# Performance work log

Measured on AMD Instinct MI355X. Metric: run time of the kernel, lower is better.

The kernel has to match this reference:

```python
import jax, jax.numpy as jnp
import numpy as np

L = 8          # curve control points per chunk (self.l)
TS = 256       # curve spatial resolution (self.ts)


def setup_inputs() -> dict:
    key = jax.random.key(0)
    k1, k2 = jax.random.split(key)
    # full-resolution input image, values in [0,1)
    x = jax.random.uniform(k1, (4, 3, 1024, 1024), dtype=jnp.float32)
    # predicted curve parameters: 9*L = 72 channels at TS x TS
    param = jax.random.normal(k2, (4, 72, TS, TS), dtype=jnp.float32)
    return {"x": x, "param": param}


def _grid_sample_3d(vol, gx, gy, gz):
    """F.grid_sample(vol, grid, 'bilinear', 'border', align_corners=True)
    vol: [B,C,D,Hc,Wc]; gx,gy,gz: [B,H,W] normalized coords in [-1,1].
    Returns [B,H,W,C] (channels last)."""
    B, C, D, Hc, Wc = vol.shape
    # align_corners=True unnormalization + border padding (clamp coords)
    ix = jnp.clip((gx + 1.0) * 0.5 * (Wc - 1), 0.0, Wc - 1)
    iy = jnp.clip((gy + 1.0) * 0.5 * (Hc - 1), 0.0, Hc - 1)
    iz = jnp.clip((gz + 1.0) * 0.5 * (D - 1), 0.0, D - 1)
    x0f, y0f, z0f = jnp.floor(ix), jnp.floor(iy), jnp.floor(iz)
    wx, wy, wz = ix - x0f, iy - y0f, iz - z0f
    x0 = x0f.astype(jnp.int32); x1 = jnp.minimum(x0 + 1, Wc - 1)
    y0 = y0f.astype(jnp.int32); y1 = jnp.minimum(y0 + 1, Hc - 1)
    z0 = z0f.astype(jnp.int32); z1 = jnp.minimum(z0 + 1, D - 1)
    vol_t = vol.transpose(0, 2, 3, 4, 1)  # [B,D,Hc,Wc,C]
    b = jnp.arange(B)[:, None, None]      # [B,1,1]
    out = jnp.zeros(gx.shape + (C,), dtype=vol.dtype)
    for zi, wz_ in ((z0, 1.0 - wz), (z1, wz)):
        for yi, wy_ in ((y0, 1.0 - wy), (y1, wy)):
            for xi, wx_ in ((x0, 1.0 - wx), (x1, wx)):
                w = (wz_ * wy_ * wx_)[..., None]          # [B,H,W,1]
                out = out + w * vol_t[b, zi, yi, xi]      # gather -> [B,H,W,C]
    return out


def reference(x, param):
    # eval-mode forward of Generator.mapping + tanh (param precomputed by CNN)
    B, _, H, W = x.shape
    Hc, Wc = param.shape[-2], param.shape[-1]
    # torch.stack(torch.chunk(param,3,dim=1),dim=1) == reshape [B,3,3L,Hc,Wc]
    curve = param.reshape(B, 3, 3 * L, Hc, Wc)
    coordh = jnp.linspace(-1.0, 1.0, H, dtype=x.dtype)[:, None]  # varies over H
    coordw = jnp.linspace(-1.0, 1.0, W, dtype=x.dtype)[None, :]  # varies over W
    gx = jnp.broadcast_to(coordw, (B, H, W))
    gy = jnp.broadcast_to(coordh, (B, H, W))
    out = jnp.zeros((B, H, W, 3), dtype=x.dtype)
    for i in range(3):  # three curve chunks, z-coordinate = i-th color channel
        curve_i = curve[:, :, i * L:(i + 1) * L]          # [B,3,L,Hc,Wc]
        out = out + _grid_sample_3d(curve_i, gx, gy, x[:, i])
    return jnp.tanh(out.transpose(0, 3, 1, 2))            # [B,3,H,W]
```

## Files before the change

### kernel.cpp

```cpp
#include <hip/hip_runtime.h>
#include <math.h>

#define IMG 1024
#define HW (IMG * IMG)
#define TS 256
#define CH_STRIDE (TS * TS)
#define PARAM_B_STRIDE (72 * CH_STRIDE)
#define S_CONST (255.0f / 1023.0f)

#define ROWS 6
#define CELLS 34
#define CELL_DW 73
#define ROW_DW (CELLS * CELL_DW)
#define LDS_DW (ROWS * ROW_DW)
#define RUNS (ROWS * 72)
#define STAGE_DW (RUNS * CELLS)

__global__ __launch_bounds__(1024, 8) void curve3d_fused(
    const float* __restrict__ x, const float* __restrict__ param,
    float* __restrict__ out)
{
    __shared__ float sh[LDS_DW];
    int blk = blockIdx.x;
    blk = (blk & 7) * 256 + (blk >> 3);
    int wt = blk & 7;
    int ht = (blk >> 3) & 63;
    int b  = blk >> 9;
    int tid = threadIdx.x;

    int w0 = wt * 128, h0 = ht * 16;
    int xb = (int)((float)w0 * S_CONST);
    int yb = (int)((float)h0 * S_CONST);

    int tw = tid & 127, th = tid >> 7;
    int w = w0 + tw;
    int ha = h0 + th;
    const float* xp = x + (size_t)b * 3 * HW + (size_t)ha * IMG + w;
    float xv[2][3];
#pragma unroll
    for (int i = 0; i < 3; ++i) {
        xv[0][i] = __builtin_nontemporal_load(xp + (size_t)i * HW);
        xv[1][i] = __builtin_nontemporal_load(xp + (size_t)i * HW + 8 * IMG);
    }

    const float* pb = param + (size_t)b * PARAM_B_STRIDE;
#pragma unroll
    for (int j = 0; j < 15; ++j) {
        int idx = tid + j * 1024;
        if (j < 14 || idx < STAGE_DW) {
            int run = idx / CELLS;
            int off = idx - run * CELLS;
            int row = run / 72;
            int ch  = run - row * 72;
            int ys = min(yb + row, 255);
            int xs = min(xb + off, 255);
            sh[row * ROW_DW + off * CELL_DW + ch] =
                pb[(size_t)ch * CH_STRIDE + ys * TS + xs];
        }
    }

    int zi[2][3]; float wz[2][3];
#pragma unroll
    for (int p = 0; p < 2; ++p)
#pragma unroll
        for (int i = 0; i < 3; ++i) {
            float f = fminf(fmaxf(fmaf(xv[p][i], 3.5f, 3.5f), 0.0f), 7.0f);
            int z = min((int)f, 6);
            zi[p][i] = z;
            wz[p][i] = f - (float)z;
        }

    __syncthreads();

    float ixf = (float)w * S_CONST; int x0 = (int)ixf; float wx = ixf - (float)x0;
    int cb0 = (x0 - xb) * CELL_DW;
    int cb1 = (min(x0 + 1, 255) - xb) * CELL_DW;
    float u0 = 1.0f - wx;

    float* op = out + (size_t)b * 3 * HW + (size_t)ha * IMG + w;

#pragma unroll
    for (int p = 0; p < 2; ++p) {
        int h = ha + p * 8;
        float iyf = (float)h * S_CONST; int y0 = (int)iyf; float wy = iyf - (float)y0;
        int rb0 = (y0 - yb) * ROW_DW;
        int rb1 = (min(y0 + 1, 255) - yb) * ROW_DW;
        float v0 = 1.0f - wy;
        float wcs[4] = {v0 * u0, v0 * wx, wy * u0, wy * wx};
        int bofs[4] = {rb0 + cb0, rb0 + cb1, rb1 + cb0, rb1 + cb1};
        float* opp = op + (size_t)(p * 8) * IMG;
#pragma unroll
        for (int c = 0; c < 3; ++c) {
            float acc = 0.0f;
#pragma unroll
            for (int i = 0; i < 3; ++i) {
                int off = (c * 3 + i) * 8 + zi[p][i];
                float wzi = wz[p][i];
#pragma unroll
                for (int k = 0; k < 4; ++k) {
                    float2 v;
                    __builtin_memcpy(&v, &sh[bofs[k] + off], 8);
                    float wb = wcs[k] * wzi;
                    float wa = wcs[k] - wb;
                    acc = fmaf(v.x, wa, fmaf(v.y, wb, acc));
                }
            }
            float e = __expf(2.0f * acc);
            __builtin_nontemporal_store(1.0f - 2.0f / (e + 1.0f),
                                        opp + (size_t)c * HW);
        }
    }
}

extern "C" void kernel_launch(void* const* d_in, const int* in_sizes, int n_in,
                              void* d_out, int out_size, void* d_ws, size_t ws_size,
                              hipStream_t stream) {
    const float* x = (const float*)d_in[0];
    const float* param = (const float*)d_in[1];
    float* out = (float*)d_out;
    curve3d_fused<<<dim3(4 * 64 * 8), dim3(1024), 0, stream>>>(x, param, out);
}
```

Measured before the change: 181.2 us.

## Remap thread tiling, restructure param staging and reorder LDS interpolation loop

Threads are remapped so each wavefront covers a 16x4 pixel patch instead of a 64-wide row strip, which should reduce LDS bank conflicts and spread accesses across cells. Param staging now uses 32-wide coalesced row loads plus a small tail for the last two columns, which removes the per-element integer division. The interpolation loop is reordered to compute the z-lerp once per corner and accumulate all three output channels together. Output stores switch from nontemporal to regular stores, which may change cache behavior.

```diff
diff --git a/kernel.cpp b/kernel.cpp
--- a/kernel.cpp
+++ b/kernel.cpp
@@ -14,7 +14,6 @@
 #define ROW_DW (CELLS * CELL_DW)
 #define LDS_DW (ROWS * ROW_DW)
 #define RUNS (ROWS * 72)
-#define STAGE_DW (RUNS * CELLS)
 
 __global__ __launch_bounds__(1024, 8) void curve3d_fused(
     const float* __restrict__ x, const float* __restrict__ param,
@@ -32,9 +31,15 @@
     int xb = (int)((float)w0 * S_CONST);
     int yb = (int)((float)h0 * S_CONST);
 
-    int tw = tid & 127, th = tid >> 7;
+    int wx = tid & 15;
+    int wyl = (tid >> 4) & 3;
+    int pxp = (tid >> 6) & 7;
+    int pyp = tid >> 9;
+    int tw = pxp * 16 + wx;
+    int th = pyp * 4 + wyl;
     int w = w0 + tw;
     int ha = h0 + th;
+
     const float* xp = x + (size_t)b * 3 * HW + (size_t)ha * IMG + w;
     float xv[2][3];
 #pragma unroll
@@ -44,19 +49,30 @@
     }
 
     const float* pb = param + (size_t)b * PARAM_B_STRIDE;
+    {
+        int off = tid & 31;
+        int g = tid >> 5;
 #pragma unroll
-    for (int j = 0; j < 15; ++j) {
-        int idx = tid + j * 1024;
-        if (j < 14 || idx < STAGE_DW) {
-            int run = idx / CELLS;
-            int off = idx - run * CELLS;
-            int row = run / 72;
-            int ch  = run - row * 72;
-            int ys = min(yb + row, 255);
-            int xs = min(xb + off, 255);
-            sh[row * ROW_DW + off * CELL_DW + ch] =
-                pb[(size_t)ch * CH_STRIDE + ys * TS + xs];
+        for (int j = 0; j < 14; ++j) {
+            int run = g + j * 32;
+            if (run < RUNS) {
+                unsigned row = (unsigned)run / 72u;
+                int ch = run - (int)row * 72;
+                int ys = min(yb + (int)row, 255);
+                sh[(int)row * ROW_DW + off * CELL_DW + ch] =
+                    pb[(size_t)ch * CH_STRIDE + ys * TS + (xb + off)];
+            }
         }
+    }
+    if (tid < 2 * RUNS) {
+        int run = tid >> 1;
+        int xx = 32 + (tid & 1);
+        unsigned row = (unsigned)run / 72u;
+        int ch = run - (int)row * 72;
+        int ys = min(yb + (int)row, 255);
+        int xs = min(xb + xx, 255);
+        sh[(int)row * ROW_DW + xx * CELL_DW + ch] =
+            pb[(size_t)ch * CH_STRIDE + ys * TS + xs];
     }
 
     int zi[2][3]; float wz[2][3];
@@ -72,42 +88,46 @@
 
     __syncthreads();
 
-    float ixf = (float)w * S_CONST; int x0 = (int)ixf; float wx = ixf - (float)x0;
+    float ixf = (float)w * S_CONST; int x0 = (int)ixf; float wxf = ixf - (float)x0;
     int cb0 = (x0 - xb) * CELL_DW;
     int cb1 = (min(x0 + 1, 255) - xb) * CELL_DW;
-    float u0 = 1.0f - wx;
+    float u0 = 1.0f - wxf;
 
     float* op = out + (size_t)b * 3 * HW + (size_t)ha * IMG + w;
 
 #pragma unroll
     for (int p = 0; p < 2; ++p) {
         int h = ha + p * 8;
-        float iyf = (float)h * S_CONST; int y0 = (int)iyf; float wy = iyf - (float)y0;
+        float iyf = (float)h * S_CONST; int y0 = (int)iyf; float wyf = iyf - (float)y0;
         int rb0 = (y0 - yb) * ROW_DW;
         int rb1 = (min(y0 + 1, 255) - yb) * ROW_DW;
-        float v0 = 1.0f - wy;
-        float wcs[4] = {v0 * u0, v0 * wx, wy * u0, wy * wx};
+        float v0 = 1.0f - wyf;
+        float wcs[4] = {v0 * u0, v0 * wxf, wyf * u0, wyf * wxf};
         int bofs[4] = {rb0 + cb0, rb0 + cb1, rb1 + cb0, rb1 + cb1};
+
+        float acc[3] = {0.0f, 0.0f, 0.0f};
+#pragma unroll
+        for (int i = 0; i < 3; ++i) {
+            float wzi = wz[p][i];
+            const float* bi = sh + zi[p][i];
+#pragma unroll
+            for (int k = 0; k < 4; ++k) {
+                const float* bp = bi + bofs[k];
+                float wk = wcs[k];
+#pragma unroll
+                for (int c = 0; c < 3; ++c) {
+                    float2 v;
+                    __builtin_memcpy(&v, bp + (c * 3 + i) * 8, 8);
+                    float t = fmaf(wzi, v.y - v.x, v.x);
+                    acc[c] = fmaf(wk, t, acc[c]);
+                }
+            }
+        }
         float* opp = op + (size_t)(p * 8) * IMG;
 #pragma unroll
         for (int c = 0; c < 3; ++c) {
-            float acc = 0.0f;
-#pragma unroll
-            for (int i = 0; i < 3; ++i) {
-                int off = (c * 3 + i) * 8 + zi[p][i];
-                float wzi = wz[p][i];
-#pragma unroll
-                for (int k = 0; k < 4; ++k) {
-                    float2 v;
-                    __builtin_memcpy(&v, &sh[bofs[k] + off], 8);
-                    float wb = wcs[k] * wzi;
-                    float wa = wcs[k] - wb;
-                    acc = fmaf(v.x, wa, fmaf(v.y, wb, acc));
-                }
-            }
-            float e = __expf(2.0f * acc);
-            __builtin_nontemporal_store(1.0f - 2.0f / (e + 1.0f),
-                                        opp + (size_t)c * HW);
+            float e = __expf(2.0f * acc[c]);
+            opp[(size_t)c * HW] = 1.0f - 2.0f / (e + 1.0f);
         }
     }
 }
```

New measurement: 177.9 us. No clear change (-1.8%).
